# Optimization experiments

Measured on AMD Instinct MI355X. Metric: run time of the kernel, lower is better.

## Reference

```python
import jax, jax.numpy as jnp
import numpy as np

N_NODES = 50000
N_EDGES = 640000
IN_SIZE = 512
HID1 = 128


def setup_inputs() -> dict:
    key = jax.random.key(0)
    ks = jax.random.split(key, 7)
    x = jax.random.normal(ks[0], (N_NODES, IN_SIZE), dtype=jnp.float32)
    edge_index = jax.random.randint(ks[1], (2, N_EDGES), 0, N_NODES, dtype=jnp.int64)
    # Linear params stored as (in, out) so y = x @ W + b (equiv to torch x @ W.T + b)
    s_enc = 1.0 / np.sqrt(IN_SIZE)
    s_dec = 1.0 / np.sqrt(HID1)
    W_enc = jax.random.uniform(ks[2], (IN_SIZE, HID1), jnp.float32, -s_enc, s_enc)
    b_enc = jax.random.uniform(ks[3], (HID1,), jnp.float32, -s_enc, s_enc)
    W_dec = jax.random.uniform(ks[4], (HID1, IN_SIZE), jnp.float32, -s_dec, s_dec)
    b_dec = jax.random.uniform(ks[5], (IN_SIZE,), jnp.float32, -s_dec, s_dec)
    gcn_bias = jnp.zeros((HID1,), dtype=jnp.float32)  # reset_parameters zeroes it
    return {"x": x, "W_enc": W_enc, "b_enc": b_enc, "W_dec": W_dec,
            "b_dec": b_dec, "gcn_bias": gcn_bias, "edge_index": edge_index}


def gcn_conv(h, edge_index, bias):
    # GCNConv with lin.weight frozen to identity (in==out), so lin is a no-op.
    N = h.shape[0]
    loops = jnp.arange(N, dtype=edge_index.dtype)
    row = jnp.concatenate([edge_index[0], loops])  # source nodes (x_j)
    col = jnp.concatenate([edge_index[1], loops])  # target nodes (aggregation)
    deg = jax.ops.segment_sum(jnp.ones_like(col, dtype=h.dtype), col, num_segments=N)
    dinv = jnp.where(deg > 0, jax.lax.rsqrt(deg), jnp.zeros_like(deg))
    norm = dinv[row] * dinv[col]              # [E+N]
    msg = norm[:, None] * h[row]              # gather + scale, [E+N, HID1]
    out = jax.ops.segment_sum(msg, col, num_segments=N)  # scatter-add
    return out + bias


def reference(x, W_enc, b_enc, W_dec, b_dec, gcn_bias, edge_index):
    encoded = jax.nn.relu(x @ W_enc + b_enc)          # [N, HID1]
    messaged = gcn_conv(encoded, edge_index, gcn_bias)
    decoded = jax.nn.sigmoid(messaged @ W_dec + b_dec)  # [N, IN_SIZE]
    return decoded
```

## Files before the change

### kernel.cpp

```cpp
#include <hip/hip_runtime.h>
#include <math.h>

#define NNODES 50000
#define NEDGES 640000
#define INSZ 512
#define HID 128
#define NBLK ((NNODES + 255) / 256)

typedef short s16x8 __attribute__((ext_vector_type(8)));
typedef float f32x4 __attribute__((ext_vector_type(4)));

static __device__ inline short f2bf(float f) {
    __bf16 b = (__bf16)f;
    return __builtin_bit_cast(short, b);
}
static __device__ inline float bf2f(unsigned short u) {
    unsigned int i = (unsigned int)u << 16;
    return __builtin_bit_cast(float, i);
}

__global__ __launch_bounds__(256) void prep_wenc(const float* __restrict__ W,
                                                 short* __restrict__ WT) {
    int t = blockIdx.x * 256 + threadIdx.x;
    if (t < INSZ * HID) {
        int n = t & (HID - 1);
        int k = t >> 7;
        WT[n * INSZ + k] = f2bf(W[t]);
    }
}
__global__ __launch_bounds__(256) void prep_wdec(const float* __restrict__ W,
                                                 short* __restrict__ WT) {
    int t = blockIdx.x * 256 + threadIdx.x;
    if (t < HID * INSZ) {
        int n = t & (INSZ - 1);
        int k = t >> 9;
        WT[n * HID + k] = f2bf(W[t]);
    }
}

__global__ __launch_bounds__(256) void count_kernel(const int* __restrict__ col,
                                                    int* __restrict__ counts) {
    int e = blockIdx.x * blockDim.x + threadIdx.x;
    if (e < NEDGES) atomicAdd(&counts[col[e]], 1);
}

__global__ __launch_bounds__(256) void partial_kernel(const int* __restrict__ counts,
                                                      int* __restrict__ blocksums) {
    int i = blockIdx.x * 256 + threadIdx.x;
    int v = (i < NNODES) ? counts[i] : 0;
#pragma unroll
    for (int off = 32; off; off >>= 1) v += __shfl_down(v, off, 64);
    __shared__ int ws[4];
    if ((threadIdx.x & 63) == 0) ws[threadIdx.x >> 6] = v;
    __syncthreads();
    if (threadIdx.x == 0) blocksums[blockIdx.x] = ws[0] + ws[1] + ws[2] + ws[3];
}

__global__ __launch_bounds__(256) void scan_blocks(const int* __restrict__ blocksums,
                                                   int* __restrict__ blockoffs) {
    __shared__ int s[256];
    const int t = threadIdx.x;
    s[t] = (t < NBLK) ? blocksums[t] : 0;
    __syncthreads();
    for (int off = 1; off < 256; off <<= 1) {
        int u = (t >= off) ? s[t - off] : 0;
        __syncthreads();
        s[t] += u;
        __syncthreads();
    }
    blockoffs[t] = (t == 0) ? 0 : s[t - 1];
}

__global__ __launch_bounds__(256) void scan_final(const int* __restrict__ counts,
                                                  const int* __restrict__ blockoffs,
                                                  int* __restrict__ starts,
                                                  int* __restrict__ cursor,
                                                  float* __restrict__ dinv) {
    __shared__ int s[256];
    const int t = threadIdx.x;
    const int i = blockIdx.x * 256 + t;
    int v = (i < NNODES) ? counts[i] : 0;
    s[t] = v;
    __syncthreads();
    for (int off = 1; off < 256; off <<= 1) {
        int u = (t >= off) ? s[t - off] : 0;
        __syncthreads();
        s[t] += u;
        __syncthreads();
    }
    int excl = ((t == 0) ? 0 : s[t - 1]) + blockoffs[blockIdx.x];
    if (i < NNODES) {
        starts[i] = excl;
        cursor[i] = excl;
        dinv[i] = rsqrtf((float)v + 1.0f);
        if (i == NNODES - 1) starts[NNODES] = excl + v;
    }
}

__global__ __launch_bounds__(256) void scatter_kernel(const int* __restrict__ erow,
                                                      const int* __restrict__ ecol,
                                                      int* __restrict__ cursor,
                                                      int* __restrict__ csr_row) {
    int e = blockIdx.x * blockDim.x + threadIdx.x;
    if (e < NEDGES) {
        int pos = atomicAdd(&cursor[ecol[e]], 1);
        csr_row[pos] = erow[e];
    }
}

#define XPAD 72
__global__ __launch_bounds__(256) void encoder_mfma(const float* __restrict__ x,
                                                    const short* __restrict__ WT,
                                                    const float* __restrict__ b,
                                                    unsigned short* __restrict__ h) {
    __shared__ short xs[2][64 * XPAD];
    const int t    = threadIdx.x;
    const int lane = t & 63;
    const int wv   = t >> 6;
    const int r16  = lane & 15;
    const int kg   = lane >> 4;
    const int mbase = blockIdx.x * 64;
    const int nb    = wv * 32;

    const float4* sp[4];
    int sdst[4];
#pragma unroll
    for (int j = 0; j < 4; ++j) {
        int c = j * 256 + t;
        int row = c >> 4, c4 = c & 15;
        int gr = mbase + row; if (gr >= NNODES) gr = NNODES - 1;
        sp[j]   = (const float4*)x + (size_t)gr * (INSZ / 4) + c4;
        sdst[j] = row * XPAD + c4 * 4;
    }

    f32x4 acc[4][2] = {};
    float4 rB[4], rC[4];

    {
        float4 rA[4];
#pragma unroll
        for (int j = 0; j < 4; ++j) rA[j] = sp[j][0];
#pragma unroll
        for (int j = 0; j < 4; ++j) {
            short4 w;
            w.x = f2bf(rA[j].x); w.y = f2bf(rA[j].y);
            w.z = f2bf(rA[j].z); w.w = f2bf(rA[j].w);
            *(short4*)&xs[0][sdst[j]] = w;
        }
    }
    __syncthreads();
#pragma unroll
    for (int j = 0; j < 4; ++j) rB[j] = sp[j][16];

#pragma unroll 2
    for (int ks = 0; ks < 8; ++ks) {
        const int cur = ks & 1;
        if (ks < 6) {
#pragma unroll
            for (int j = 0; j < 4; ++j) rC[j] = sp[j][(ks + 2) * 16];
        }
#pragma unroll
        for (int kk = 0; kk < 2; ++kk) {
            s16x8 a[4], bb[2];
#pragma unroll
            for (int mt = 0; mt < 4; ++mt)
                a[mt] = *(const s16x8*)&xs[cur][(mt * 16 + r16) * XPAD + kk * 32 + kg * 8];
#pragma unroll
            for (int nt = 0; nt < 2; ++nt)
                bb[nt] = *(const s16x8*)(WT + (size_t)(nb + nt * 16 + r16) * INSZ + ks * 64 + kk * 32 + kg * 8);
#pragma unroll
            for (int mt = 0; mt < 4; ++mt)
#pragma unroll
                for (int nt = 0; nt < 2; ++nt)
                    acc[mt][nt] = __builtin_amdgcn_mfma_f32_16x16x32_bf16(a[mt], bb[nt], acc[mt][nt], 0, 0, 0);
        }
        if (ks < 7) {
#pragma unroll
            for (int j = 0; j < 4; ++j) {
                short4 w;
                w.x = f2bf(rB[j].x); w.y = f2bf(rB[j].y);
                w.z = f2bf(rB[j].z); w.w = f2bf(rB[j].w);
                *(short4*)&xs[cur ^ 1][sdst[j]] = w;
            }
#pragma unroll
            for (int j = 0; j < 4; ++j) rB[j] = rC[j];
        }
        __syncthreads();
    }

    const int ro = kg * 4;
#pragma unroll
    for (int mt = 0; mt < 4; ++mt) {
        const int row0 = mbase + mt * 16 + ro;
#pragma unroll
        for (int nt = 0; nt < 2; ++nt) {
            const int col = nb + nt * 16 + r16;
            const float bj = b[col];
#pragma unroll
            for (int v = 0; v < 4; ++v) {
                int rr = row0 + v;
                if (rr < NNODES)
                    h[(size_t)rr * HID + col] = (unsigned short)f2bf(fmaxf(acc[mt][nt][v] + bj, 0.0f));
            }
        }
    }
}

__global__ __launch_bounds__(256) void aggregate_csr_kernel(const int* __restrict__ starts,
                                                            const int* __restrict__ csr_row,
                                                            const float* __restrict__ dinv,
                                                            const unsigned short* __restrict__ h,
                                                            unsigned short* __restrict__ agg) {
    const int node = (blockIdx.x * 256 + threadIdx.x) >> 5;
    const int l32  = threadIdx.x & 31;
    if (node >= NNODES) return;
    const float dc = dinv[node];
    const int s0 = starts[node], s1 = starts[node + 1];
    const ushort4* hp = (const ushort4*)h;

    ushort4 sv = hp[(size_t)node * 32 + l32];
    const float sc = dc * dc;
    float4 acc;
    acc.x = bf2f(sv.x) * sc; acc.y = bf2f(sv.y) * sc;
    acc.z = bf2f(sv.z) * sc; acc.w = bf2f(sv.w) * sc;

    int i = s0;
    for (; i + 3 < s1; i += 4) {
        int r0 = csr_row[i], r1 = csr_row[i + 1], r2 = csr_row[i + 2], r3 = csr_row[i + 3];
        float n0 = dinv[r0] * dc, n1 = dinv[r1] * dc, n2 = dinv[r2] * dc, n3 = dinv[r3] * dc;
        ushort4 h0 = hp[(size_t)r0 * 32 + l32];
        ushort4 h1 = hp[(size_t)r1 * 32 + l32];
        ushort4 h2 = hp[(size_t)r2 * 32 + l32];
        ushort4 h3 = hp[(size_t)r3 * 32 + l32];
        acc.x = fmaf(n0, bf2f(h0.x), acc.x); acc.y = fmaf(n0, bf2f(h0.y), acc.y);
        acc.z = fmaf(n0, bf2f(h0.z), acc.z); acc.w = fmaf(n0, bf2f(h0.w), acc.w);
        acc.x = fmaf(n1, bf2f(h1.x), acc.x); acc.y = fmaf(n1, bf2f(h1.y), acc.y);
        acc.z = fmaf(n1, bf2f(h1.z), acc.z); acc.w = fmaf(n1, bf2f(h1.w), acc.w);
        acc.x = fmaf(n2, bf2f(h2.x), acc.x); acc.y = fmaf(n2, bf2f(h2.y), acc.y);
        acc.z = fmaf(n2, bf2f(h2.z), acc.z); acc.w = fmaf(n2, bf2f(h2.w), acc.w);
        acc.x = fmaf(n3, bf2f(h3.x), acc.x); acc.y = fmaf(n3, bf2f(h3.y), acc.y);
        acc.z = fmaf(n3, bf2f(h3.z), acc.z); acc.w = fmaf(n3, bf2f(h3.w), acc.w);
    }
    for (; i < s1; ++i) {
        int r = csr_row[i];
        float nrm = dinv[r] * dc;
        ushort4 hv = hp[(size_t)r * 32 + l32];
        acc.x = fmaf(nrm, bf2f(hv.x), acc.x); acc.y = fmaf(nrm, bf2f(hv.y), acc.y);
        acc.z = fmaf(nrm, bf2f(hv.z), acc.z); acc.w = fmaf(nrm, bf2f(hv.w), acc.w);
    }
    ushort4 ov;
    ov.x = (unsigned short)f2bf(acc.x); ov.y = (unsigned short)f2bf(acc.y);
    ov.z = (unsigned short)f2bf(acc.z); ov.w = (unsigned short)f2bf(acc.w);
    ((ushort4*)agg)[(size_t)node * 32 + l32] = ov;
}

#define APAD 136
#define EPAD 68
__global__ __launch_bounds__(512) void decoder_mfma(const unsigned short* __restrict__ agg,
                                                    const float* __restrict__ gb,
                                                    const short* __restrict__ WT,
                                                    const float* __restrict__ b,
                                                    float* __restrict__ out) {
    __shared__ short as_lds[64 * APAD];
    __shared__ float ep[8][16 * EPAD];
    const int t    = threadIdx.x;
    const int lane = t & 63;
    const int wv   = t >> 6;
    const int r16  = lane & 15;
    const int kg   = lane >> 4;
    const int mbase = blockIdx.x * 64;
    const int nwb   = wv * 64;

    {
        const int row = t >> 3;
        const int f0  = (t & 7) * 16;
        int gr = mbase + row; if (gr >= NNODES) gr = NNODES - 1;
        const ushort4* src4 = (const ushort4*)(agg + (size_t)gr * HID + f0);
        const float4*  g4   = (const float4*)(gb + f0);
        short4* d4 = (short4*)(as_lds + row * APAD + f0);
#pragma unroll
        for (int j = 0; j < 4; ++j) {
            ushort4 u = src4[j];
            float4 g = g4[j];
            short4 w;
            w.x = f2bf(bf2f(u.x) + g.x); w.y = f2bf(bf2f(u.y) + g.y);
            w.z = f2bf(bf2f(u.z) + g.z); w.w = f2bf(bf2f(u.w) + g.w);
            d4[j] = w;
        }
    }
    __syncthreads();

    f32x4 acc[4][4] = {};
#pragma unroll
    for (int ks = 0; ks < 4; ++ks) {
        s16x8 a[4], bb[4];
#pragma unroll
        for (int mt = 0; mt < 4; ++mt)
            a[mt] = *(const s16x8*)&as_lds[(mt * 16 + r16) * APAD + ks * 32 + kg * 8];
#pragma unroll
        for (int nt = 0; nt < 4; ++nt)
            bb[nt] = *(const s16x8*)(WT + (size_t)(nwb + nt * 16 + r16) * HID + ks * 32 + kg * 8);
#pragma unroll
        for (int mt = 0; mt < 4; ++mt)
#pragma unroll
            for (int nt = 0; nt < 4; ++nt)
                acc[mt][nt] = __builtin_amdgcn_mfma_f32_16x16x32_bf16(a[mt], bb[nt], acc[mt][nt], 0, 0, 0);
    }

    float bj[4];
#pragma unroll
    for (int nt = 0; nt < 4; ++nt) bj[nt] = b[nwb + nt * 16 + r16];

    float* eps = ep[wv];
#pragma unroll
    for (int mt = 0; mt < 4; ++mt) {
#pragma unroll
        for (int nt = 0; nt < 4; ++nt)
#pragma unroll
            for (int v = 0; v < 4; ++v) {
                float z = acc[mt][nt][v] + bj[nt];
                eps[(kg * 4 + v) * EPAD + nt * 16 + r16] = 1.0f / (1.0f + __expf(-z));
            }
#pragma unroll
        for (int pass = 0; pass < 4; ++pass) {
            const int lr = pass * 4 + kg;
            float4 vv = *(const float4*)&eps[lr * EPAD + r16 * 4];
            const int rr = mbase + mt * 16 + lr;
            if (rr < NNODES)
                *(float4*)&out[(size_t)rr * INSZ + nwb + r16 * 4] = vv;
        }
    }
}

extern "C" void kernel_launch(void* const* d_in, const int* in_sizes, int n_in,
                              void* d_out, int out_size, void* d_ws, size_t ws_size,
                              hipStream_t stream) {
    const float* x        = (const float*)d_in[0];
    const float* W_enc    = (const float*)d_in[1];
    const float* b_enc    = (const float*)d_in[2];
    const float* W_dec    = (const float*)d_in[3];
    const float* b_dec    = (const float*)d_in[4];
    const float* gcn_bias = (const float*)d_in[5];
    const int*   edge     = (const int*)d_in[6];
    const int*   erow = edge;
    const int*   ecol = edge + NEDGES;

    float* out = (float*)d_out;
    unsigned short* agg = (unsigned short*)d_ws;
    float* dinv  = (float*)(agg + (size_t)NNODES * HID);
    short* wdecT = (short*)(dinv + NNODES);
    unsigned short* h = (unsigned short*)out;
    int*   csr_row   = (int*)(out + (size_t)NNODES * HID);
    int*   starts    = csr_row + NEDGES;
    int*   counts    = starts + NNODES + 1;
    int*   cursor    = counts + NNODES;
    int*   blocksums = cursor + NNODES;
    int*   blockoffs = blocksums + 256;
    short* wencT     = (short*)(blockoffs + 256);

    hipMemsetAsync(counts, 0, (size_t)NNODES * sizeof(int), stream);
    prep_wenc<<<(INSZ * HID + 255) / 256, 256, 0, stream>>>(W_enc, wencT);
    prep_wdec<<<(HID * INSZ + 255) / 256, 256, 0, stream>>>(W_dec, wdecT);
    count_kernel<<<(NEDGES + 255) / 256, 256, 0, stream>>>(ecol, counts);
    partial_kernel<<<NBLK, 256, 0, stream>>>(counts, blocksums);
    scan_blocks<<<1, 256, 0, stream>>>(blocksums, blockoffs);
    scan_final<<<NBLK, 256, 0, stream>>>(counts, blockoffs, starts, cursor, dinv);
    scatter_kernel<<<(NEDGES + 255) / 256, 256, 0, stream>>>(erow, ecol, cursor, csr_row);
    encoder_mfma<<<(NNODES + 63) / 64, 256, 0, stream>>>(x, wencT, b_enc, h);
    aggregate_csr_kernel<<<((size_t)NNODES * 32 + 255) / 256, 256, 0, stream>>>(starts, csr_row, dinv, h, agg);
    decoder_mfma<<<(NNODES + 63) / 64, 512, 0, stream>>>(agg, gcn_bias, wdecT, b_dec, out);
}
```

Baseline: 190.0 us.

## Fuse CSR build into one cooperative kernel and merge weight prep

Replaces the memset, count, partial-sum, block-scan, final-scan and scatter kernels with a single cooperative kernel that separates the phases with grid-wide syncs. The two weight transpose/convert kernels are merged into one launch. The aim is to cut kernel-launch count and inter-kernel gaps. In exchange, the edge loops now run on only about 196 blocks, and each grid.sync has its own cost.

```diff
diff --git a/kernel.cpp b/kernel.cpp
--- a/kernel.cpp
+++ b/kernel.cpp
@@ -1,5 +1,8 @@
 #include <hip/hip_runtime.h>
+#include <hip/hip_cooperative_groups.h>
 #include <math.h>
+
+namespace cg = cooperative_groups;
 
 #define NNODES 50000
 #define NEDGES 640000
@@ -19,67 +22,45 @@
     return __builtin_bit_cast(float, i);
 }
 
-__global__ __launch_bounds__(256) void prep_wenc(const float* __restrict__ W,
-                                                 short* __restrict__ WT) {
+__global__ __launch_bounds__(256) void prep_weights(const float* __restrict__ We,
+                                                    const float* __restrict__ Wd,
+                                                    short* __restrict__ WTe,
+                                                    short* __restrict__ WTd) {
     int t = blockIdx.x * 256 + threadIdx.x;
     if (t < INSZ * HID) {
         int n = t & (HID - 1);
         int k = t >> 7;
-        WT[n * INSZ + k] = f2bf(W[t]);
-    }
-}
-__global__ __launch_bounds__(256) void prep_wdec(const float* __restrict__ W,
-                                                 short* __restrict__ WT) {
-    int t = blockIdx.x * 256 + threadIdx.x;
-    if (t < HID * INSZ) {
-        int n = t & (INSZ - 1);
-        int k = t >> 9;
-        WT[n * HID + k] = f2bf(W[t]);
-    }
-}
-
-__global__ __launch_bounds__(256) void count_kernel(const int* __restrict__ col,
-                                                    int* __restrict__ counts) {
-    int e = blockIdx.x * blockDim.x + threadIdx.x;
-    if (e < NEDGES) atomicAdd(&counts[col[e]], 1);
-}
-
-__global__ __launch_bounds__(256) void partial_kernel(const int* __restrict__ counts,
-                                                      int* __restrict__ blocksums) {
-    int i = blockIdx.x * 256 + threadIdx.x;
-    int v = (i < NNODES) ? counts[i] : 0;
-#pragma unroll
-    for (int off = 32; off; off >>= 1) v += __shfl_down(v, off, 64);
-    __shared__ int ws[4];
-    if ((threadIdx.x & 63) == 0) ws[threadIdx.x >> 6] = v;
-    __syncthreads();
-    if (threadIdx.x == 0) blocksums[blockIdx.x] = ws[0] + ws[1] + ws[2] + ws[3];
-}
-
-__global__ __launch_bounds__(256) void scan_blocks(const int* __restrict__ blocksums,
-                                                   int* __restrict__ blockoffs) {
-    __shared__ int s[256];
-    const int t = threadIdx.x;
-    s[t] = (t < NBLK) ? blocksums[t] : 0;
-    __syncthreads();
-    for (int off = 1; off < 256; off <<= 1) {
-        int u = (t >= off) ? s[t - off] : 0;
-        __syncthreads();
-        s[t] += u;
-        __syncthreads();
-    }
-    blockoffs[t] = (t == 0) ? 0 : s[t - 1];
-}
-
-__global__ __launch_bounds__(256) void scan_final(const int* __restrict__ counts,
-                                                  const int* __restrict__ blockoffs,
-                                                  int* __restrict__ starts,
-                                                  int* __restrict__ cursor,
-                                                  float* __restrict__ dinv) {
-    __shared__ int s[256];
+        WTe[n * INSZ + k] = f2bf(We[t]);
+    } else {
+        int u = t - INSZ * HID;
+        int n = u & (INSZ - 1);
+        int k = u >> 9;
+        WTd[n * HID + k] = f2bf(Wd[u]);
+    }
+}
+
+__global__ __launch_bounds__(256) void csr_build(const int* __restrict__ erow,
+                                                 const int* __restrict__ ecol,
+                                                 int* __restrict__ counts,
+                                                 int* __restrict__ starts,
+                                                 int* __restrict__ cursor,
+                                                 float* __restrict__ dinv,
+                                                 int* __restrict__ csr_row,
+                                                 int* __restrict__ blocksums) {
+    cg::grid_group grid = cg::this_grid();
     const int t = threadIdx.x;
     const int i = blockIdx.x * 256 + t;
-    int v = (i < NNODES) ? counts[i] : 0;
+    const int gsz = NBLK * 256;
+
+    if (i < NNODES) counts[i] = 0;
+    grid.sync();
+
+    for (int e = i; e < NEDGES; e += gsz)
+        atomicAdd(&counts[ecol[e]], 1);
+    grid.sync();
+
+    __shared__ int s[256];
+    const int v = (i < NNODES) ? counts[i] : 0;
     s[t] = v;
     __syncthreads();
     for (int off = 1; off < 256; off <<= 1) {
@@ -88,21 +69,36 @@
         s[t] += u;
         __syncthreads();
     }
-    int excl = ((t == 0) ? 0 : s[t - 1]) + blockoffs[blockIdx.x];
     if (i < NNODES) {
+        starts[i] = (t == 0) ? 0 : s[t - 1];
+        dinv[i] = rsqrtf((float)v + 1.0f);
+    }
+    if (t == 255) blocksums[blockIdx.x] = s[255];
+    grid.sync();
+
+    if (blockIdx.x == 0) {
+        int bv = (t < NBLK) ? blocksums[t] : 0;
+        s[t] = bv;
+        __syncthreads();
+        for (int off = 1; off < 256; off <<= 1) {
+            int u = (t >= off) ? s[t - off] : 0;
+            __syncthreads();
+            s[t] += u;
+            __syncthreads();
+        }
+        if (t < NBLK) blocksums[t] = (t == 0) ? 0 : s[t - 1];
+    }
+    grid.sync();
+
+    if (i < NNODES) {
+        int excl = starts[i] + blocksums[blockIdx.x];
         starts[i] = excl;
         cursor[i] = excl;
-        dinv[i] = rsqrtf((float)v + 1.0f);
         if (i == NNODES - 1) starts[NNODES] = excl + v;
     }
-}
-
-__global__ __launch_bounds__(256) void scatter_kernel(const int* __restrict__ erow,
-                                                      const int* __restrict__ ecol,
-                                                      int* __restrict__ cursor,
-                                                      int* __restrict__ csr_row) {
-    int e = blockIdx.x * blockDim.x + threadIdx.x;
-    if (e < NEDGES) {
+    grid.sync();
+
+    for (int e = i; e < NEDGES; e += gsz) {
         int pos = atomicAdd(&cursor[ecol[e]], 1);
         csr_row[pos] = erow[e];
     }
@@ -355,17 +351,17 @@
     int*   counts    = starts + NNODES + 1;
     int*   cursor    = counts + NNODES;
     int*   blocksums = cursor + NNODES;
-    int*   blockoffs = blocksums + 256;
-    short* wencT     = (short*)(blockoffs + 256);
-
-    hipMemsetAsync(counts, 0, (size_t)NNODES * sizeof(int), stream);
-    prep_wenc<<<(INSZ * HID + 255) / 256, 256, 0, stream>>>(W_enc, wencT);
-    prep_wdec<<<(HID * INSZ + 255) / 256, 256, 0, stream>>>(W_dec, wdecT);
-    count_kernel<<<(NEDGES + 255) / 256, 256, 0, stream>>>(ecol, counts);
-    partial_kernel<<<NBLK, 256, 0, stream>>>(counts, blocksums);
-    scan_blocks<<<1, 256, 0, stream>>>(blocksums, blockoffs);
-    scan_final<<<NBLK, 256, 0, stream>>>(counts, blockoffs, starts, cursor, dinv);
-    scatter_kernel<<<(NEDGES + 255) / 256, 256, 0, stream>>>(erow, ecol, cursor, csr_row);
+    short* wencT     = (short*)(blocksums + 256);
+
+    prep_weights<<<(2 * INSZ * HID + 255) / 256, 256, 0, stream>>>(W_enc, W_dec, wencT, wdecT);
+
+    int*   counts_a = counts;  int* starts_a = starts;  int* cursor_a = cursor;
+    float* dinv_a = dinv;      int* csr_a = csr_row;    int* bs_a = blocksums;
+    const int* erow_a = erow;  const int* ecol_a = ecol;
+    void* args[] = {(void*)&erow_a, (void*)&ecol_a, (void*)&counts_a, (void*)&starts_a,
+                    (void*)&cursor_a, (void*)&dinv_a, (void*)&csr_a, (void*)&bs_a};
+    hipLaunchCooperativeKernel((void*)csr_build, dim3(NBLK), dim3(256), args, 0, stream);
+
     encoder_mfma<<<(NNODES + 63) / 64, 256, 0, stream>>>(x, wencT, b_enc, h);
     aggregate_csr_kernel<<<((size_t)NNODES * 32 + 255) / 256, 256, 0, stream>>>(starts, csr_row, dinv, h, agg);
     decoder_mfma<<<(NNODES + 63) / 64, 512, 0, stream>>>(agg, gcn_bias, wdecT, b_dec, out);
```

Result: slower. 290.1 us (+52.7%).
